# Kernel tuning notes

Hardware: AMD Instinct MI355X
Metric: run time of the kernel (lower is better)

## Reference

```python
import jax, jax.numpy as jnp
import numpy as np

D_HEAD = 64      # per-head dim (init d_head)
WINDOW = 64      # sliding_window_size
ROPE_BASE = 10000.0


def _rope(x):
    # x: [B, H, L, d] ; standard half-split rotary embedding over positions 0..L-1
    L, d = x.shape[-2], x.shape[-1]
    half = d // 2
    inv_freq = 1.0 / (ROPE_BASE ** (jnp.arange(half, dtype=jnp.float32) / half))
    ang = jnp.arange(L, dtype=jnp.float32)[:, None] * inv_freq  # [L, half]
    cos, sin = jnp.cos(ang), jnp.sin(ang)
    x1, x2 = x[..., :half], x[..., half:]
    return jnp.concatenate([x1 * cos - x2 * sin, x1 * sin + x2 * cos], axis=-1)


def setup_inputs() -> dict:
    key = jax.random.key(0)
    ks = jax.random.split(key, 4)
    B, L, D, H = 4, 2048, 2048, 2048
    nh = H // D_HEAD
    S = 16  # num_sinks
    u = jax.random.normal(ks[0], (B, L, D), jnp.float32)
    Wqkv = jax.random.normal(ks[1], (3 * H, D), jnp.float32) / np.sqrt(D)
    bqkv = jnp.zeros((3 * H,), jnp.float32)
    Wo = jax.random.normal(ks[2], (D, H), jnp.float32) / np.sqrt(H)
    bo = jnp.zeros((D,), jnp.float32)
    sinks = jax.random.normal(ks[3], (nh, S, D_HEAD), jnp.float32) / np.sqrt(D_HEAD)
    return {"u": u, "Wqkv": Wqkv, "bqkv": bqkv, "Wo": Wo, "bo": bo, "sinks": sinks}


def reference(u, Wqkv, bqkv, Wo, bo, sinks):
    B, L, D = u.shape
    d, w = D_HEAD, WINDOW
    nh, S, _ = sinks.shape
    scale = 1.0 / np.sqrt(d)

    qkv = u @ Wqkv.T + bqkv                         # [B, L, 3H]
    q, k, v = jnp.split(qkv, 3, axis=-1)
    heads = lambda x: x.reshape(B, L, nh, d).transpose(0, 2, 1, 3)  # [B, nh, L, d]
    q, k, v = heads(q), heads(k), heads(v)
    q, k = _rope(q), _rope(k)

    # Banded (sliding-window) attention in blocks of size w: query block i
    # attends key blocks {i-1, i, i+1} plus S global sink tokens.
    # Sink queries (prepended in the original) are discarded by O[:, :, -L:],
    # so we only compute attention for the L real queries.
    nb = L // w
    Qb = q.reshape(B, nh, nb, w, d)
    Kb = k.reshape(B, nh, nb, w, d)
    Vb = v.reshape(B, nh, nb, w, d)

    blk = jnp.arange(nb)[:, None] + jnp.arange(-1, 2)[None, :]   # [nb, 3]
    valid = (blk >= 0) & (blk < nb)
    blkc = jnp.clip(blk, 0, nb - 1)
    Kband = Kb[:, :, blkc].reshape(B, nh, nb, 3 * w, d)
    Vband = Vb[:, :, blkc].reshape(B, nh, nb, 3 * w, d)

    qpos = (jnp.arange(nb) * w)[:, None] + jnp.arange(w)          # [nb, w]
    kpos = ((blkc * w)[..., None] + jnp.arange(w)).reshape(nb, 3 * w)
    vmask = jnp.broadcast_to(valid[:, :, None], (nb, 3, w)).reshape(nb, 3 * w)
    mask = vmask[:, None, :] & (jnp.abs(qpos[:, :, None] - kpos[:, None, :]) <= w)  # [nb, w, 3w]

    s_band = jnp.einsum('bhnqd,bhnkd->bhnqk', Qb, Kband) * scale
    s_band = jnp.where(mask, s_band, -jnp.inf)
    s_sink = jnp.einsum('bhnqd,hsd->bhnqs', Qb, sinks) * scale    # sink K = sink param (no RoPE)
    p = jax.nn.softmax(jnp.concatenate([s_sink, s_band], axis=-1), axis=-1)

    O = (jnp.einsum('bhnqs,hsd->bhnqd', p[..., :S], sinks)        # sink V = sink param
         + jnp.einsum('bhnqk,bhnkd->bhnqd', p[..., S:], Vband))
    y = O.reshape(B, nh, L, d).transpose(0, 2, 1, 3).reshape(B, L, nh * d)
    return y @ Wo.T + bo
```

## Files before the change

kernel.cpp:

```cpp
#include <hip/hip_runtime.h>
#include <hip/hip_bf16.h>

typedef unsigned short u16;
typedef __attribute__((ext_vector_type(8))) short bf16x8;
typedef __attribute__((ext_vector_type(4))) float f32x4;

__device__ __forceinline__ u16 f2b(float f) {
  union { __hip_bfloat16 h; u16 u; } cv;
  cv.h = __float2bfloat16(f);
  return cv.u;
}
__device__ __forceinline__ float b2f(u16 u) {
  union { unsigned int i; float f; } cv;
  cv.i = ((unsigned int)u) << 16;
  return cv.f;
}

__global__ void cvt_bf16(const float* __restrict__ in, u16* __restrict__ out) {
  size_t i = ((size_t)blockIdx.x * 256 + threadIdx.x) * 4;
  float4 v = *(const float4*)(in + i);
  ushort4 o;
  o.x = f2b(v.x); o.y = f2b(v.y); o.z = f2b(v.z); o.w = f2b(v.w);
  *(ushort4*)(out + i) = o;
}

__global__ void rope_tab_k(float2* __restrict__ tab) {
  int t = blockIdx.x * 256 + threadIdx.x;
  int l = t >> 5, i = t & 31;
  float inv = powf(10000.0f, -(float)i * (1.0f / 32.0f));
  float ang = (float)l * inv;
  tab[t] = make_float2(cosf(ang), sinf(ang));
}

template<int NCOLS, bool ROPE>
__global__ __launch_bounds__(512, 2) void gemm_p(const u16* __restrict__ A,
                                                 const u16* __restrict__ Bm,
                                                 const float* __restrict__ bias,
                                                 u16* __restrict__ Cb,
                                                 float* __restrict__ Cf,
                                                 const float2* __restrict__ tab) {
  extern __shared__ char smem[];
  u16* Asl = (u16*)smem;
  u16* Bsl = (u16*)(smem + 65536);
  const int tid = threadIdx.x, lane = tid & 63, w = tid >> 6;
  const int wr = w >> 2, wcn = w & 3;
  const int fr = lane & 15, fk = lane >> 4;
  const int m0 = blockIdx.y * 256, n0 = blockIdx.x * 256;
  const int srow = lane >> 2;
  const int gslot = (lane & 3) ^ ((lane >> 3) & 3);
  const int c0 = w * 2, c1 = c0 + 1;
  const int sel = (fr >> 1) & 3;
  const int ka = (fk ^ sel) << 4;
  f32x4 acc[8][4] = {};

  auto stage = [&](int jj) {
    int slot = jj & 3;
    int kk = jj * 32 + gslot * 8;
    u16* Ad = Asl + slot * 8192;
    u16* Bd = Bsl + slot * 8192;
    const u16* gA0 = A  + (size_t)(m0 + c0 * 16 + srow) * 2048 + kk;
    const u16* gA1 = A  + (size_t)(m0 + c1 * 16 + srow) * 2048 + kk;
    const u16* gB0 = Bm + (size_t)(n0 + c0 * 16 + srow) * 2048 + kk;
    const u16* gB1 = Bm + (size_t)(n0 + c1 * 16 + srow) * 2048 + kk;
    __builtin_amdgcn_global_load_lds((const __attribute__((address_space(1))) unsigned int*)gA0,
        (__attribute__((address_space(3))) unsigned int*)(Ad + c0 * 512), 16, 0, 0);
    __builtin_amdgcn_global_load_lds((const __attribute__((address_space(1))) unsigned int*)gA1,
        (__attribute__((address_space(3))) unsigned int*)(Ad + c1 * 512), 16, 0, 0);
    __builtin_amdgcn_global_load_lds((const __attribute__((address_space(1))) unsigned int*)gB0,
        (__attribute__((address_space(3))) unsigned int*)(Bd + c0 * 512), 16, 0, 0);
    __builtin_amdgcn_global_load_lds((const __attribute__((address_space(1))) unsigned int*)gB1,
        (__attribute__((address_space(3))) unsigned int*)(Bd + c1 * 512), 16, 0, 0);
  };

  stage(0); stage(1); stage(2);
  asm volatile("s_waitcnt vmcnt(8)" ::: "memory");
  asm volatile("s_barrier" ::: "memory");

  for (int j = 0; j < 64; ++j) {
    if (j < 61) stage(j + 3);
    const char* Ab = (const char*)(Asl + (j & 3) * 8192);
    const char* Bb = (const char*)(Bsl + (j & 3) * 8192);
    bf16x8 af[8], bv[4];
    #pragma unroll
    for (int m = 0; m < 8; ++m)
      af[m] = *(const bf16x8*)(Ab + (wr * 128 + m * 16 + fr) * 64 + ka);
    #pragma unroll
    for (int n = 0; n < 4; ++n)
      bv[n] = *(const bf16x8*)(Bb + (wcn * 64 + n * 16 + fr) * 64 + ka);
    __builtin_amdgcn_s_setprio(1);
    #pragma unroll
    for (int m = 0; m < 8; ++m)
      #pragma unroll
      for (int n = 0; n < 4; ++n)
        acc[m][n] = __builtin_amdgcn_mfma_f32_16x16x32_bf16(af[m], bv[n], acc[m][n], 0, 0, 0);
    __builtin_amdgcn_s_setprio(0);
    if (j < 61)       asm volatile("s_waitcnt vmcnt(8)" ::: "memory");
    else if (j == 61) asm volatile("s_waitcnt vmcnt(4)" ::: "memory");
    else if (j == 62) asm volatile("s_waitcnt vmcnt(0)" ::: "memory");
    asm volatile("s_waitcnt lgkmcnt(0)" ::: "memory");
    asm volatile("s_barrier" ::: "memory");
  }

  #pragma unroll
  for (int m = 0; m < 8; ++m) {
    int grow0 = m0 + wr * 128 + m * 16 + fk * 4;
    #pragma unroll
    for (int n = 0; n < 4; ++n) {
      int gcol = n0 + wcn * 64 + n * 16 + fr;
      if (ROPE) {
        if (gcol < 4096) {
          int c = gcol & 63;
          int i = c & 31;
          bool lo = c < 32;
          float bx = bias[gcol], bp = bias[gcol ^ 32];
          #pragma unroll
          for (int r = 0; r < 4; ++r) {
            int t = grow0 + r;
            float2 cs = tab[((t & 2047) << 5) + i];
            float xb = acc[m][n][r] + bx;
            float pb = acc[m][n ^ 2][r] + bp;
            float o = lo ? (xb * cs.x - pb * cs.y) : (pb * cs.y + xb * cs.x);
            Cb[(size_t)t * NCOLS + gcol] = f2b(o);
          }
        } else {
          float bx = bias[gcol];
          #pragma unroll
          for (int r = 0; r < 4; ++r)
            Cb[(size_t)(grow0 + r) * NCOLS + gcol] = f2b(acc[m][n][r] + bx);
        }
      } else {
        float bx = bias[gcol];
        #pragma unroll
        for (int r = 0; r < 4; ++r)
          Cf[(size_t)(grow0 + r) * NCOLS + gcol] = acc[m][n][r] + bx;
      }
    }
  }
}

#define PSTR 232
__global__ __launch_bounds__(256) void attn_k(const u16* __restrict__ qkv,
                                              const float* __restrict__ sinks,
                                              u16* __restrict__ O) {
  __shared__ char smem[59392];
  char* Kraw = smem;
  char* Qraw = smem + 28672;
  u16* Ps = (u16*)smem;
  u16* Vt = (u16*)(smem + 29696);
  const int tid = threadIdx.x, lane = tid & 63, wid = tid >> 6;
  const int fr = lane & 15, fk = lane >> 4;
  const int bx = blockIdx.x;
  const int n = bx & 31, h = (bx >> 5) & 31, b = bx >> 10;
  const size_t qrow0 = (size_t)b * 2048 + n * 64;

  for (int c = tid; c < 512; c += 256) {
    int row = c >> 3, colb = (c & 7) * 16;
    uint4 v = *(const uint4*)((const char*)(qkv + (qrow0 + row) * 6144 + h * 64) + colb);
    *(uint4*)(Qraw + ((row * 128 + colb) ^ ((row & 7) << 4))) = v;
  }
  {
    int row = tid >> 4, col4 = (tid & 15) * 4;
    float4 v = *(const float4*)(sinks + ((size_t)h * 16 + row) * 64 + col4);
    ushort4 o; o.x = f2b(v.x); o.y = f2b(v.y); o.z = f2b(v.z); o.w = f2b(v.w);
    *(ushort4*)(Kraw + ((row * 128 + col4 * 2) ^ ((row & 7) << 4))) = o;
  }
  for (int c = tid; c < 1536; c += 256) {
    int kidx = c >> 3, colb = (c & 7) * 16;
    int blk = n - 1 + (kidx >> 6);
    int blkc = min(max(blk, 0), 31);
    int kpos = blkc * 64 + (kidx & 63);
    uint4 v = *(const uint4*)((const char*)(qkv + ((size_t)b * 2048 + kpos) * 6144 + 2048 + h * 64) + colb);
    int row = 16 + kidx;
    *(uint4*)(Kraw + ((row * 128 + colb) ^ ((row & 7) << 4))) = v;
  }
  if (tid < 128) {
    int row = 208 + (tid >> 3), colb = (tid & 7) * 16;
    uint4 z = {0, 0, 0, 0};
    *(uint4*)(Kraw + ((row * 128 + colb) ^ ((row & 7) << 4))) = z;
  }
  __syncthreads();

  bf16x8 qf[2];
  {
    int qrow = wid * 16 + fr;
    #pragma unroll
    for (int kc = 0; kc < 2; ++kc)
      qf[kc] = *(const bf16x8*)(Qraw + ((qrow * 128 + kc * 64 + fk * 16) ^ ((qrow & 7) << 4)));
  }
  f32x4 sacc[14];
  #pragma unroll
  for (int g = 0; g < 14; ++g) {
    int key = g * 16 + fr;
    bf16x8 kf0 = *(const bf16x8*)(Kraw + ((key * 128 + fk * 16) ^ ((key & 7) << 4)));
    bf16x8 kf1 = *(const bf16x8*)(Kraw + ((key * 128 + 64 + fk * 16) ^ ((key & 7) << 4)));
    f32x4 a = {};
    a = __builtin_amdgcn_mfma_f32_16x16x32_bf16(qf[0], kf0, a, 0, 0, 0);
    a = __builtin_amdgcn_mfma_f32_16x16x32_bf16(qf[1], kf1, a, 0, 0, 0);
    sacc[g] = a;
  }
  float rowmax[4] = {-3e38f, -3e38f, -3e38f, -3e38f};
  #pragma unroll
  for (int g = 0; g < 14; ++g) {
    int key = g * 16 + fr;
    #pragma unroll
    for (int r = 0; r < 4; ++r) {
      float s = sacc[g][r] * 0.125f;
      bool valid;
      if (key < 16) valid = true;
      else if (key < 208) {
        int kidx = key - 16;
        int blk = n - 1 + (kidx >> 6);
        int kpos = blk * 64 + (kidx & 63);
        int qpos = n * 64 + wid * 16 + fk * 4 + r;
        valid = (blk >= 0) && (blk < 32) && (qpos - kpos <= 64) && (kpos - qpos <= 64);
      } else valid = false;
      s = valid ? s : -1e30f;
      sacc[g][r] = s;
      rowmax[r] = fmaxf(rowmax[r], s);
    }
  }
  #pragma unroll
  for (int d = 1; d < 16; d <<= 1)
    #pragma unroll
    for (int r = 0; r < 4; ++r)
      rowmax[r] = fmaxf(rowmax[r], __shfl_xor(rowmax[r], d));
  float rowsum[4] = {0, 0, 0, 0};
  #pragma unroll
  for (int g = 0; g < 14; ++g)
    #pragma unroll
    for (int r = 0; r < 4; ++r) {
      float p = __expf(sacc[g][r] - rowmax[r]);
      sacc[g][r] = p;
      rowsum[r] += p;
    }
  #pragma unroll
  for (int d = 1; d < 16; d <<= 1)
    #pragma unroll
    for (int r = 0; r < 4; ++r)
      rowsum[r] += __shfl_xor(rowsum[r], d);
  __syncthreads();

  #pragma unroll
  for (int g = 0; g < 14; ++g)
    #pragma unroll
    for (int r = 0; r < 4; ++r)
      Ps[(wid * 16 + fk * 4 + r) * PSTR + g * 16 + fr] = f2b(sacc[g][r]);
  {
    int dout = tid & 63, kb = tid >> 6;
    #pragma unroll
    for (int key = kb; key < 16; key += 4)
      Vt[dout * PSTR + key] = f2b(sinks[((size_t)h * 16 + key) * 64 + dout]);
    for (int kidx = kb; kidx < 192; kidx += 4) {
      int blk = n - 1 + (kidx >> 6);
      int blkc = min(max(blk, 0), 31);
      int kpos = blkc * 64 + (kidx & 63);
      Vt[dout * PSTR + 16 + kidx] = qkv[((size_t)b * 2048 + kpos) * 6144 + 4096 + h * 64 + dout];
    }
    #pragma unroll
    for (int key = 208 + kb; key < 224; key += 4)
      Vt[dout * PSTR + key] = 0;
  }
  __syncthreads();

  f32x4 oacc[4] = {};
  #pragma unroll
  for (int kc = 0; kc < 7; ++kc) {
    bf16x8 pf = *(const bf16x8*)(Ps + (wid * 16 + fr) * PSTR + kc * 32 + fk * 8);
    #pragma unroll
    for (int gd = 0; gd < 4; ++gd) {
      bf16x8 vf = *(const bf16x8*)(Vt + (gd * 16 + fr) * PSTR + kc * 32 + fk * 8);
      oacc[gd] = __builtin_amdgcn_mfma_f32_16x16x32_bf16(pf, vf, oacc[gd], 0, 0, 0);
    }
  }
  #pragma unroll
  for (int gd = 0; gd < 4; ++gd)
    #pragma unroll
    for (int r = 0; r < 4; ++r) {
      int qrl = wid * 16 + fk * 4 + r;
      float v = oacc[gd][r] / rowsum[r];
      O[(qrow0 + qrl) * 2048 + h * 64 + gd * 16 + fr] = f2b(v);
    }
}

extern "C" void kernel_launch(void* const* d_in, const int* in_sizes, int n_in,
                              void* d_out, int out_size, void* d_ws, size_t ws_size,
                              hipStream_t stream) {
  const float* u     = (const float*)d_in[0];
  const float* Wqkv  = (const float*)d_in[1];
  const float* bqkv  = (const float*)d_in[2];
  const float* Wo    = (const float*)d_in[3];
  const float* bo    = (const float*)d_in[4];
  const float* sinks = (const float*)d_in[5];
  float* out = (float*)d_out;

  char* ws = (char*)d_ws;
  u16* u_bf   = (u16*)ws;
  u16* w1_bf  = (u16*)(ws + 33554432);
  u16* qkv_bf = (u16*)(ws + 58720256);
  float2* tab = (float2*)(ws + 159383552);
  u16* O_bf  = u_bf;
  u16* w2_bf = w1_bf;

  hipFuncSetAttribute((const void*)gemm_p<6144, true>,
                      hipFuncAttributeMaxDynamicSharedMemorySize, 131072);
  hipFuncSetAttribute((const void*)gemm_p<2048, false>,
                      hipFuncAttributeMaxDynamicSharedMemorySize, 131072);

  cvt_bf16<<<16384, 256, 0, stream>>>(u, u_bf);
  cvt_bf16<<<12288, 256, 0, stream>>>(Wqkv, w1_bf);
  rope_tab_k<<<256, 256, 0, stream>>>(tab);
  gemm_p<6144, true><<<dim3(24, 32), 512, 131072, stream>>>(u_bf, w1_bf, bqkv, qkv_bf, nullptr, tab);
  attn_k<<<4096, 256, 0, stream>>>(qkv_bf, sinks, O_bf);
  cvt_bf16<<<4096, 256, 0, stream>>>(Wo, w2_bf);
  gemm_p<2048, false><<<dim3(8, 32), 512, 131072, stream>>>(O_bf, w2_bf, bo, nullptr, out, nullptr);
}
```

Measured before the change: 556.4 us.

## Vectorize V transpose via LDS staging and reorder GEMM barrier scheduling

The attention kernel now loads V rows and sinks with 16-byte vector loads. It transposes them through a per-wave LDS scratch tile into an XOR-swizzled Vt layout, replacing strided 2-byte global gathers. The read side of the PV MFMA is updated to use the swizzled addressing. Separately, the GEMM main loop moves the LDS barrier and lgkmcnt wait ahead of the MFMA block and adds sched_barriers, meant to overlap the next-stage wait with compute. Shared memory grows to 66816 bytes through dynamic allocation, which may reduce attention occupancy.

```diff
diff --git a/kernel.cpp b/kernel.cpp
--- a/kernel.cpp
+++ b/kernel.cpp
@@ -82,11 +82,14 @@
     const char* Bb = (const char*)(Bsl + (j & 3) * 8192);
     bf16x8 af[8], bv[4];
     #pragma unroll
+    for (int n = 0; n < 4; ++n)
+      bv[n] = *(const bf16x8*)(Bb + (wcn * 64 + n * 16 + fr) * 64 + ka);
+    #pragma unroll
     for (int m = 0; m < 8; ++m)
       af[m] = *(const bf16x8*)(Ab + (wr * 128 + m * 16 + fr) * 64 + ka);
-    #pragma unroll
-    for (int n = 0; n < 4; ++n)
-      bv[n] = *(const bf16x8*)(Bb + (wcn * 64 + n * 16 + fr) * 64 + ka);
+    asm volatile("s_barrier" ::: "memory");
+    asm volatile("s_waitcnt lgkmcnt(0)" ::: "memory");
+    __builtin_amdgcn_sched_barrier(0);
     __builtin_amdgcn_s_setprio(1);
     #pragma unroll
     for (int m = 0; m < 8; ++m)
@@ -94,10 +97,10 @@
       for (int n = 0; n < 4; ++n)
         acc[m][n] = __builtin_amdgcn_mfma_f32_16x16x32_bf16(af[m], bv[n], acc[m][n], 0, 0, 0);
     __builtin_amdgcn_s_setprio(0);
+    __builtin_amdgcn_sched_barrier(0);
     if (j < 61)       asm volatile("s_waitcnt vmcnt(8)" ::: "memory");
     else if (j == 61) asm volatile("s_waitcnt vmcnt(4)" ::: "memory");
     else if (j == 62) asm volatile("s_waitcnt vmcnt(0)" ::: "memory");
-    asm volatile("s_waitcnt lgkmcnt(0)" ::: "memory");
     asm volatile("s_barrier" ::: "memory");
   }
 
@@ -142,11 +145,12 @@
 __global__ __launch_bounds__(256) void attn_k(const u16* __restrict__ qkv,
                                               const float* __restrict__ sinks,
                                               u16* __restrict__ O) {
-  __shared__ char smem[59392];
+  extern __shared__ char smem[];
   char* Kraw = smem;
   char* Qraw = smem + 28672;
   u16* Ps = (u16*)smem;
   u16* Vt = (u16*)(smem + 29696);
+  char* tmpb = smem + 62464;
   const int tid = threadIdx.x, lane = tid & 63, wid = tid >> 6;
   const int fr = lane & 15, fk = lane >> 4;
   const int bx = blockIdx.x;
@@ -245,20 +249,38 @@
     #pragma unroll
     for (int r = 0; r < 4; ++r)
       Ps[(wid * 16 + fk * 4 + r) * PSTR + g * 16 + fr] = f2b(sacc[g][r]);
+
   {
-    int dout = tid & 63, kb = tid >> 6;
-    #pragma unroll
-    for (int key = kb; key < 16; key += 4)
-      Vt[dout * PSTR + key] = f2b(sinks[((size_t)h * 16 + key) * 64 + dout]);
-    for (int kidx = kb; kidx < 192; kidx += 4) {
+    u16* tw = (u16*)(tmpb + wid * 1088);
+    const int g = lane >> 3, s = lane & 7;
+    if (wid < 2) {
+      int key = wid * 8 + g;
+      float4 v0 = *(const float4*)(sinks + ((size_t)h * 16 + key) * 64 + s * 8);
+      float4 v1 = *(const float4*)(sinks + ((size_t)h * 16 + key) * 64 + s * 8 + 4);
+      u16* dst = tw + g * 68 + s * 8;
+      dst[0] = f2b(v0.x); dst[1] = f2b(v0.y); dst[2] = f2b(v0.z); dst[3] = f2b(v0.w);
+      dst[4] = f2b(v1.x); dst[5] = f2b(v1.y); dst[6] = f2b(v1.z); dst[7] = f2b(v1.w);
+      u16 col[8];
+      #pragma unroll
+      for (int k = 0; k < 8; ++k) col[k] = tw[k * 68 + lane];
+      *(bf16x8*)(Vt + lane * 256 + ((wid ^ (lane & 7)) * 8)) = *(bf16x8*)col;
+    } else {
+      bf16x8 z = {};
+      *(bf16x8*)(Vt + lane * 256 + (((24 + wid) ^ (lane & 7)) * 8)) = z;
+    }
+    for (int it = 0; it < 6; ++it) {
+      int kidx = it * 32 + wid * 8 + g;
       int blk = n - 1 + (kidx >> 6);
       int blkc = min(max(blk, 0), 31);
       int kpos = blkc * 64 + (kidx & 63);
-      Vt[dout * PSTR + 16 + kidx] = qkv[((size_t)b * 2048 + kpos) * 6144 + 4096 + h * 64 + dout];
-    }
-    #pragma unroll
-    for (int key = 208 + kb; key < 224; key += 4)
-      Vt[dout * PSTR + key] = 0;
+      uint4 v = *(const uint4*)(qkv + ((size_t)b * 2048 + kpos) * 6144 + 4096 + h * 64 + s * 8);
+      *(uint4*)(tw + g * 68 + s * 8) = v;
+      u16 col[8];
+      #pragma unroll
+      for (int k = 0; k < 8; ++k) col[k] = tw[k * 68 + lane];
+      int gi = 2 + it * 4 + wid;
+      *(bf16x8*)(Vt + lane * 256 + ((gi ^ (lane & 7)) * 8)) = *(bf16x8*)col;
+    }
   }
   __syncthreads();
 
@@ -268,7 +290,7 @@
     bf16x8 pf = *(const bf16x8*)(Ps + (wid * 16 + fr) * PSTR + kc * 32 + fk * 8);
     #pragma unroll
     for (int gd = 0; gd < 4; ++gd) {
-      bf16x8 vf = *(const bf16x8*)(Vt + (gd * 16 + fr) * PSTR + kc * 32 + fk * 8);
+      bf16x8 vf = *(const bf16x8*)(Vt + (gd * 16 + fr) * 256 + (((kc * 4 + fk) ^ (fr & 7)) * 8));
       oacc[gd] = __builtin_amdgcn_mfma_f32_16x16x32_bf16(pf, vf, oacc[gd], 0, 0, 0);
     }
   }
@@ -305,12 +327,14 @@
                       hipFuncAttributeMaxDynamicSharedMemorySize, 131072);
   hipFuncSetAttribute((const void*)gemm_p<2048, false>,
                       hipFuncAttributeMaxDynamicSharedMemorySize, 131072);
+  hipFuncSetAttribute((const void*)attn_k,
+                      hipFuncAttributeMaxDynamicSharedMemorySize, 66816);
 
   cvt_bf16<<<16384, 256, 0, stream>>>(u, u_bf);
   cvt_bf16<<<12288, 256, 0, stream>>>(Wqkv, w1_bf);
   rope_tab_k<<<256, 256, 0, stream>>>(tab);
   gemm_p<6144, true><<<dim3(24, 32), 512, 131072, stream>>>(u_bf, w1_bf, bqkv, qkv_bf, nullptr, tab);
-  attn_k<<<4096, 256, 0, stream>>>(qkv_bf, sinks, O_bf);
+  attn_k<<<4096, 256, 66816, stream>>>(qkv_bf, sinks, O_bf);
   cvt_bf16<<<4096, 256, 0, stream>>>(Wo, w2_bf);
   gemm_p<2048, false><<<dim3(8, 32), 512, 131072, stream>>>(O_bf, w2_bf, bo, nullptr, out, nullptr);
 }
```

After: 521.3 us. -6.3%, faster.
